# Kernel tuning notes

Measured on AMD Instinct MI355X. Metric: run time of the kernel, lower is better.

Reference implementation:

```python
import jax, jax.numpy as jnp
import numpy as np

KERNEL = (8, 8)
STRIDE = (4, 4)


def setup_inputs() -> dict:
    key = jax.random.key(0)
    x = jax.random.normal(key, (8, 32, 8, 8, 4096), dtype=jnp.float32)
    return {"x": x}


def reference(x):
    b, c, k1, k2, l = x.shape
    s1, s2 = STRIDE
    n = round(l ** 0.5)  # patch grid is n x n (row-major: i outer, j inner)
    h = s1 * (n - 1) + k1
    w = s2 * (n - 1) + k2
    # b c k1 k2 (n n) -> indexable per kernel offset
    xp = x.reshape(b, c, k1, k2, n, n)
    out = jnp.zeros((b, c, h, w), dtype=x.dtype)
    # For a fixed kernel offset (di, dj), the target positions p*s+di are a
    # non-overlapping strided slice, so each add is a disjoint scatter.
    for di in range(k1):
        for dj in range(k2):
            out = out.at[:, :, di:di + s1 * n:s1, dj:dj + s2 * n:s2].add(
                xp[:, :, di, dj])
    return out
```

## Files before the change

### kernel.cpp

```cpp
#include <hip/hip_runtime.h>


#define N_PATCH 64
#define L       4096
#define H_OUT   260
#define T_BLK   65
#define BC      256

__global__ __launch_bounds__(256) void fold_kernel(const float* __restrict__ x,
                                                   float* __restrict__ out) {
    int idx = blockIdx.x * blockDim.x + threadIdx.x;
    int t    = idx % T_BLK;
    int rest = idx / T_BLK;
    int h    = rest % H_OUT;
    int bc   = rest / H_OUT;

    float acc0 = 0.f, acc1 = 0.f, acc2 = 0.f, acc3 = 0.f;

    int r  = h & 3;
    int i0 = h >> 2;

    int xb = bc * (64 * L);

    #pragma unroll
    for (int p = 0; p < 2; ++p) {
        int di = r + 4 * p;
        int i  = i0 - p;
        if ((unsigned)i < (unsigned)N_PATCH) {
            int base = xb + di * (8 * L) + i * N_PATCH;
            if (t < N_PATCH) {
                int a = base + t;
                acc0 += x[a + 0 * L];
                acc1 += x[a + 1 * L];
                acc2 += x[a + 2 * L];
                acc3 += x[a + 3 * L];
            }
            if (t >= 1) {
                int a = base + t - 1;
                acc0 += x[a + 4 * L];
                acc1 += x[a + 5 * L];
                acc2 += x[a + 6 * L];
                acc3 += x[a + 7 * L];
            }
        }
    }

    int ob = (bc * H_OUT + h) * H_OUT + 4 * t;
    float4 v = make_float4(acc0, acc1, acc2, acc3);
    *reinterpret_cast<float4*>(out + ob) = v;
}

extern "C" void kernel_launch(void* const* d_in, const int* in_sizes, int n_in,
                              void* d_out, int out_size, void* d_ws, size_t ws_size,
                              hipStream_t stream) {
    const float* x = (const float*)d_in[0];
    float* out     = (float*)d_out;

    const int total  = BC * H_OUT * T_BLK;
    const int block  = 256;
    const int grid   = total / block;

    fold_kernel<<<grid, block, 0, stream>>>(x, out);
}
```

Baseline: 369.5 us.

## Stage input patches in LDS with float4 loads, one block per patch row

```diff
diff --git a/kernel.cpp b/kernel.cpp
--- a/kernel.cpp
+++ b/kernel.cpp
@@ -1,53 +1,64 @@
 #include <hip/hip_runtime.h>
 
 
-#define N_PATCH 64
-#define L       4096
-#define H_OUT   260
-#define T_BLK   65
-#define BC      256
+#define L     4096
+#define H_OUT 260
+#define NB_A  65
 
 __global__ __launch_bounds__(256) void fold_kernel(const float* __restrict__ x,
                                                    float* __restrict__ out) {
-    int idx = blockIdx.x * blockDim.x + threadIdx.x;
-    int t    = idx % T_BLK;
-    int rest = idx / T_BLK;
-    int h    = rest % H_OUT;
-    int bc   = rest / H_OUT;
+    __shared__ float lds[64 * 64];
 
-    float acc0 = 0.f, acc1 = 0.f, acc2 = 0.f, acc3 = 0.f;
+    const int bid = blockIdx.x;
+    const int a   = bid % NB_A;
+    const int bc  = bid / NB_A;
+    const int tid = threadIdx.x;
 
-    int r  = h & 3;
-    int i0 = h >> 2;
-
-    int xb = bc * (64 * L);
+    const float* xb = x + (size_t)bc * (64 * L);
 
     #pragma unroll
-    for (int p = 0; p < 2; ++p) {
-        int di = r + 4 * p;
-        int i  = i0 - p;
-        if ((unsigned)i < (unsigned)N_PATCH) {
-            int base = xb + di * (8 * L) + i * N_PATCH;
-            if (t < N_PATCH) {
-                int a = base + t;
-                acc0 += x[a + 0 * L];
-                acc1 += x[a + 1 * L];
-                acc2 += x[a + 2 * L];
-                acc3 += x[a + 3 * L];
-            }
-            if (t >= 1) {
-                int a = base + t - 1;
-                acc0 += x[a + 4 * L];
-                acc1 += x[a + 5 * L];
-                acc2 += x[a + 6 * L];
-                acc3 += x[a + 7 * L];
-            }
+    for (int q = 0; q < 4; ++q) {
+        const int c   = q * 256 + tid;
+        const int row = c >> 4;
+        const int pos = c & 15;
+        const bool lower = row < 32;
+        const int  i     = lower ? a : (a - 1);
+        const bool valid = lower ? (a < 64) : (a > 0);
+        float4 v = make_float4(0.f, 0.f, 0.f, 0.f);
+        if (valid) {
+            v = *reinterpret_cast<const float4*>(xb + row * L + i * 64 + pos * 4);
         }
+        *reinterpret_cast<float4*>(&lds[row * 64 + pos * 4]) = v;
     }
+    __syncthreads();
 
-    int ob = (bc * H_OUT + h) * H_OUT + 4 * t;
-    float4 v = make_float4(acc0, acc1, acc2, acc3);
-    *reinterpret_cast<float4*>(out + ob) = v;
+    for (int q = tid; q < 260; q += 256) {
+        const int r = q / 65;
+        const int t = q % 65;
+        const int jA = (t < 64) ? t : 63;
+        const int jB = (t > 0) ? (t - 1) : 0;
+        const float mA = (t < 64) ? 1.f : 0.f;
+        const float mB = (t > 0) ? 1.f : 0.f;
+        const float* ldsA = &lds[(r * 8) * 64];
+        const float* ldsC = &lds[((r + 4) * 8) * 64];
+        float acc[4];
+        #pragma unroll
+        for (int k = 0; k < 4; ++k) {
+            const float vA = ldsA[k * 64 + jA];
+            const float vB = ldsA[(k + 4) * 64 + jB];
+            const float vC = ldsC[k * 64 + jA];
+            const float vD = ldsC[(k + 4) * 64 + jB];
+            float s = mA * vA;
+            s += mB * vB;
+            s += mA * vC;
+            s += mB * vD;
+            acc[k] = s;
+        }
+        const int h = 4 * a + r;
+        const size_t ob = ((size_t)bc * H_OUT + h) * H_OUT + 4 * t;
+        *reinterpret_cast<float4*>(out + ob) =
+            make_float4(acc[0], acc[1], acc[2], acc[3]);
+    }
 }
 
 extern "C" void kernel_launch(void* const* d_in, const int* in_sizes, int n_in,
@@ -56,9 +67,8 @@
     const float* x = (const float*)d_in[0];
     float* out     = (float*)d_out;
 
-    const int total  = BC * H_OUT * T_BLK;
-    const int block  = 256;
-    const int grid   = total / block;
+    const int grid  = 256 * NB_A;
+    const int block = 256;
 
     fold_kernel<<<grid, block, 0, stream>>>(x, out);
 }
```

Measured after the change: 369.5 us. No clear change (+0.0%).
